# Performance work log

Measured on AMD Instinct MI355X. Metric: run time of the kernel, lower is better.

## Reference

```python
import jax, jax.numpy as jnp
import numpy as np

ORIENTATIONS = 9
CELL = 8  # pixels_per_cell


def setup_inputs() -> dict:
    key = jax.random.key(0)
    x = jax.random.normal(key, (64, 1, 512, 512), dtype=jnp.float32)
    base = jnp.array([[1.0, 0.0, -1.0], [2.0, 0.0, -2.0], [1.0, 0.0, -1.0]], dtype=jnp.float32)
    weight = jnp.stack([base, base.T])[:, None, :, :]  # [2,1,3,3]
    return {"x": x, "weight": weight}


def reference(x, weight):
    # 3x3 Sobel-like gradient conv (cross-correlation, padding=1), NCHW
    gxy = jax.lax.conv_general_dilated(
        x, weight, window_strides=(1, 1), padding=[(1, 1), (1, 1)],
        dimension_numbers=("NCHW", "OIHW", "NCHW"))  # [n,2,h,w]
    gx, gy = gxy[:, 0], gxy[:, 1]
    mag = jnp.sqrt(gx * gx + gy * gy)            # [n,h,w]
    phase = jnp.arctan2(gx, gy)                  # [n,h,w]
    phase_int = phase / jnp.pi * ORIENTATIONS
    fl = jnp.floor(phase_int).astype(jnp.int32) % ORIENTATIONS
    ce = jnp.ceil(phase_int).astype(jnp.int32) % ORIENTATIONS
    # scatter_(set into zeros) + scatter_add_ == sum of two weighted one-hots
    hist = (jax.nn.one_hot(fl, ORIENTATIONS, dtype=mag.dtype)
            + jax.nn.one_hot(ce, ORIENTATIONS, dtype=mag.dtype)) * mag[..., None]  # [n,h,w,O]
    out = jnp.transpose(hist, (0, 3, 1, 2))      # [n,O,h,w]
    n, o, h, w = out.shape
    # avg_pool2d with kernel==stride==CELL
    pooled = out.reshape(n, o, h // CELL, CELL, w // CELL, CELL).mean(axis=(3, 5))
    return pooled.reshape(n, -1)  # feature_vector=True
```

## Files before the change

### kernel.cpp

```cpp
#include <hip/hip_runtime.h>
#include <math.h>


#define IMH 512
#define IMW 512
#define NCELLS (64 * 64 * 64)

#define F32(h) __builtin_bit_cast(float, (unsigned)(h))
__device__ __forceinline__ unsigned fbits(float f) { return __builtin_bit_cast(unsigned, f); }
__device__ __forceinline__ int mod9(int b) { int r = b % 9; return r < 0 ? r + 9 : r; }

__device__ float fd_atanf_fma(float x) {
#pragma clang fp contract(off)
    unsigned hx = fbits(x);
    unsigned ix = hx & 0x7fffffffu;
    if (ix >= 0x4c800000u) {
        if (ix > 0x7f800000u) return x + x;
        float r = F32(0x3fc90fda) + F32(0x33a22168);
        return (hx >> 31) ? -r : r;
    }
    int id;
    if (ix < 0x3ee00000u) {
        if (ix < 0x39800000u) return x;
        id = -1;
    } else {
        x = fabsf(x);
        if (ix < 0x3f980000u) {
            if (ix < 0x3f300000u) { id = 0; x = fmaf(2.0f, x, -1.0f) / (2.0f + x); }
            else                  { id = 1; x = (x - 1.0f) / (x + 1.0f); }
        } else {
            if (ix < 0x401c0000u) { id = 2; x = (x - 1.5f) / fmaf(1.5f, x, 1.0f); }
            else                  { id = 3; x = -1.0f / x; }
        }
    }
    float z = x * x;
    float w = z * z;
    float s1 = z * fmaf(w, fmaf(w, F32(0x3d7cac25), F32(0x3e11f50d)), F32(0x3eaaaaa3));
    float s2 = w * fmaf(w, F32(0xbdda1247), F32(0xbe4cca98));
    if (id < 0) return fmaf(-x, s1 + s2, x);
    float hi = (id == 0) ? F32(0x3eed6338) : (id == 1) ? F32(0x3f490fda)
             : (id == 2) ? F32(0x3f7b985e) : F32(0x3fc90fda);
    float lo = (id == 0) ? F32(0x31ac3769) : (id == 1) ? F32(0x33222168)
             : (id == 2) ? F32(0x33140fb4) : F32(0x33a22168);
    float zz = hi - (fmaf(x, s1 + s2, -lo) - x);
    return (hx >> 31) ? -zz : zz;
}

__device__ float fd_atan2f_fma(float y, float x) {
#pragma clang fp contract(off)
    unsigned hx = fbits(x), hy = fbits(y);
    unsigned ix = hx & 0x7fffffffu, iy = hy & 0x7fffffffu;
    const float pi     = F32(0x40490fdb);
    const float pi_lo  = F32(0xb3bbbd2e);
    const float pi_o_2 = F32(0x3fc90fdb);
    if (hx == 0x3f800000u) return fd_atanf_fma(y);
    unsigned m = ((hy >> 31) & 1u) | ((hx >> 30) & 2u);
    if (iy == 0u) {
        switch (m) {
            case 0: case 1: return y;
            case 2: return pi;
            default: return -pi;
        }
    }
    if (ix == 0u) return (hy >> 31) ? -pi_o_2 : pi_o_2;
    int k = ((int)iy - (int)ix) >> 23;
    float z;
    unsigned mm = m;
    if (k > 26) {
        z = pi_o_2 + 0.5f * pi_lo;
        mm = m & 1u;
    } else if (k < -26 && (hx >> 31)) {
        z = 0.0f;
    } else {
        z = fd_atanf_fma(fabsf(y / x));
    }
    switch (mm) {
        case 0:  return z;
        case 1:  return -z;
        case 2:  return pi - (z - pi_lo);
        default: return (z - pi_lo) - pi;
    }
}

__global__ __launch_bounds__(256) void hog_kernel(const float* __restrict__ x,
                                                  float* __restrict__ out) {
#pragma clang fp contract(off)
    const int wid  = threadIdx.x >> 6;
    const int lane = threadIdx.x & 63;
    const int cell = blockIdx.x * 4 + wid;
    const int n  = cell >> 12;
    const int ch = (cell >> 6) & 63;
    const int cw = cell & 63;
    const int py = lane >> 3;
    const int px = lane & 7;
    const int h = (ch << 3) + py;
    const int w = (cw << 3) + px;

    const float* xn = x + (size_t)n * (IMH * IMW);

    float v[3][3];
#pragma unroll
    for (int dy = 0; dy < 3; ++dy) {
#pragma unroll
        for (int dx = 0; dx < 3; ++dx) {
            int hh = h + dy - 1;
            int ww = w + dx - 1;
            bool ok = ((unsigned)hh < (unsigned)IMH) && ((unsigned)ww < (unsigned)IMW);
            v[dy][dx] = ok ? xn[hh * IMW + ww] : 0.0f;
        }
    }

    float gx = v[0][0];
    gx = gx - v[0][2];
    gx = gx + 2.0f * v[1][0];
    gx = gx - 2.0f * v[1][2];
    gx = gx + v[2][0];
    gx = gx - v[2][2];

    float gy = v[0][0];
    gy = gy + 2.0f * v[0][1];
    gy = gy + v[0][2];
    gy = gy - v[2][0];
    gy = gy - 2.0f * v[2][1];
    gy = gy - v[2][2];

    float m2f = gx * gx + gy * gy;
    float mag = sqrtf(m2f);

    float Sx = fabsf(v[0][0]) + fabsf(v[0][2])
             + 2.0f * (fabsf(v[1][0]) + fabsf(v[1][2]))
             + fabsf(v[2][0]) + fabsf(v[2][2]);
    float Sy = fabsf(v[0][0]) + fabsf(v[2][0])
             + 2.0f * (fabsf(v[0][1]) + fabsf(v[2][1]))
             + fabsf(v[0][2]) + fabsf(v[2][2]);

    float ph32 = atan2f(gx, gy);
    float t32 = (ph32 / F32(0x40490fdb)) * 9.0f;
    float agx = fabsf(gx), agy = fabsf(gy);
    float Eph32 = 3.0e-7f * fabsf(ph32) + 1e-12f;
    if (m2f > 0.0f)
        Eph32 += (agy * (3.6e-7f * Sx) + agx * (3.6e-7f * Sy)) / m2f;
    float Et32 = 2.8648f * Eph32 + 3.6e-7f * fmaxf(fabsf(t32), 1.0f)
               + 3.5e-8f * fabsf(t32);
    float d32 = fabsf(t32 - rintf(t32));

    int b0 = 0, b1 = 0, b2 = 0;
    float w0 = 0.0f, w1 = 0.0f, w2 = 0.0f;

    if (d32 > 4.0f * Et32 && m2f > 0.0f) {
        int k0 = (int)floorf(t32);
        b0 = mod9(k0); b1 = mod9(k0 + 1);
        w0 = mag; w1 = mag;
    } else {
        double gx64 = ((double)v[0][0] - (double)v[0][2])
                    + 2.0 * ((double)v[1][0] - (double)v[1][2])
                    + ((double)v[2][0] - (double)v[2][2]);
        double gy64 = ((double)v[0][0] - (double)v[2][0])
                    + 2.0 * ((double)v[0][1] - (double)v[2][1])
                    + ((double)v[0][2] - (double)v[2][2]);
        double m2 = gx64 * gx64 + gy64 * gy64;
        if (m2 == 0.0) {
            b0 = 0; b1 = 0; w0 = mag; w1 = mag;
        } else {
            double ph = atan2(gx64, gy64);
            double t64 = (ph / 3.14159274101257324) * 9.0;
            double dgx = 2.4e-7 * (double)Sx;
            double dgy = 2.4e-7 * (double)Sy;
            double dpa = (fabs(gy64) * dgx + fabs(gx64) * dgy) / m2;
            double dpi = 2.4e-7 * fabs(ph) + 1e-30;
            double E = 2.86479 * (dpa + dpi)
                     + 1.8e-7 * fmax(fabs(t64), 1.0)
                     + 3.5e-8 * fabs(t64);
            double kd = floor(t64 + 0.5);
            double d = fabs(t64 - kd);
            int k = (int)kd;
            if (d <= E) {
                if (mag <= 8.3f) {
                    b0 = mod9(k - 1); b1 = mod9(k); b2 = mod9(k + 1);
                    w0 = 0.5f * mag; w1 = 1.5f * mag; w2 = 0.5f * mag;
                } else {
                    float phf = fd_atan2f_fma(gx, gy);
                    float tf = (phf / F32(0x40490fdb)) * 9.0f;
                    int fl = (int)floorf(tf);
                    int ce = (int)ceilf(tf);
                    b0 = mod9(fl); b1 = mod9(ce);
                    w0 = mag; w1 = mag;
                }
            } else {
                int k0 = (int)floor(t64);
                b0 = mod9(k0); b1 = mod9(k0 + 1);
                w0 = mag; w1 = mag;
            }
        }
    }

    float myband = 0.0f;
#pragma unroll
    for (int o = 0; o < 9; ++o) {
        float s = (b0 == o ? w0 : 0.0f) + (b1 == o ? w1 : 0.0f) + (b2 == o ? w2 : 0.0f);
#pragma unroll
        for (int d = 1; d < 64; d <<= 1) {
            s += __shfl_xor(s, d, 64);
        }
        if (lane == o) myband = s;
    }

    if (lane < 9) {
        out[(((size_t)n * 9 + lane) * 64 + ch) * 64 + cw] = myband * (1.0f / 64.0f);
    }
}

extern "C" void kernel_launch(void* const* d_in, const int* in_sizes, int n_in,
                              void* d_out, int out_size, void* d_ws, size_t ws_size,
                              hipStream_t stream) {
    const float* x = (const float*)d_in[0];
    float* out = (float*)d_out;
    const int blocks = NCELLS / 4;
    hog_kernel<<<blocks, 256, 0, stream>>>(x, out);
}
```

Before: 226.7 us.

## Stage input strips in LDS and accumulate cell histograms with shared atomics

```diff
diff --git a/kernel.cpp b/kernel.cpp
--- a/kernel.cpp
+++ b/kernel.cpp
@@ -4,7 +4,10 @@
 
 #define IMH 512
 #define IMW 512
-#define NCELLS (64 * 64 * 64)
+#define STRIP 32
+#define ROWS 10
+#define COLS (STRIP * 8 + 2)
+#define RS 261
 
 #define F32(h) __builtin_bit_cast(float, (unsigned)(h))
 __device__ __forceinline__ unsigned fbits(float f) { return __builtin_bit_cast(unsigned, f); }
@@ -85,128 +88,147 @@
 __global__ __launch_bounds__(256) void hog_kernel(const float* __restrict__ x,
                                                   float* __restrict__ out) {
 #pragma clang fp contract(off)
-    const int wid  = threadIdx.x >> 6;
-    const int lane = threadIdx.x & 63;
-    const int cell = blockIdx.x * 4 + wid;
-    const int n  = cell >> 12;
-    const int ch = (cell >> 6) & 63;
-    const int cw = cell & 63;
-    const int py = lane >> 3;
-    const int px = lane & 7;
-    const int h = (ch << 3) + py;
-    const int w = (cw << 3) + px;
+    __shared__ float tile[ROWS * RS];
+    __shared__ float hist[STRIP * 9];
+
+    const int tid = threadIdx.x;
+    const int bid = blockIdx.x;
+    const int n  = bid >> 7;
+    const int ch = (bid & 127) >> 1;
+    const int s  = bid & 1;
+    const int cw0px = s * (STRIP * 8);
 
     const float* xn = x + (size_t)n * (IMH * IMW);
 
-    float v[3][3];
-#pragma unroll
-    for (int dy = 0; dy < 3; ++dy) {
-#pragma unroll
-        for (int dx = 0; dx < 3; ++dx) {
-            int hh = h + dy - 1;
-            int ww = w + dx - 1;
-            bool ok = ((unsigned)hh < (unsigned)IMH) && ((unsigned)ww < (unsigned)IMW);
-            v[dy][dx] = ok ? xn[hh * IMW + ww] : 0.0f;
-        }
-    }
-
-    float gx = v[0][0];
-    gx = gx - v[0][2];
-    gx = gx + 2.0f * v[1][0];
-    gx = gx - 2.0f * v[1][2];
-    gx = gx + v[2][0];
-    gx = gx - v[2][2];
-
-    float gy = v[0][0];
-    gy = gy + 2.0f * v[0][1];
-    gy = gy + v[0][2];
-    gy = gy - v[2][0];
-    gy = gy - 2.0f * v[2][1];
-    gy = gy - v[2][2];
-
-    float m2f = gx * gx + gy * gy;
-    float mag = sqrtf(m2f);
-
-    float Sx = fabsf(v[0][0]) + fabsf(v[0][2])
-             + 2.0f * (fabsf(v[1][0]) + fabsf(v[1][2]))
-             + fabsf(v[2][0]) + fabsf(v[2][2]);
-    float Sy = fabsf(v[0][0]) + fabsf(v[2][0])
-             + 2.0f * (fabsf(v[0][1]) + fabsf(v[2][1]))
-             + fabsf(v[0][2]) + fabsf(v[2][2]);
-
-    float ph32 = atan2f(gx, gy);
-    float t32 = (ph32 / F32(0x40490fdb)) * 9.0f;
-    float agx = fabsf(gx), agy = fabsf(gy);
-    float Eph32 = 3.0e-7f * fabsf(ph32) + 1e-12f;
-    if (m2f > 0.0f)
-        Eph32 += (agy * (3.6e-7f * Sx) + agx * (3.6e-7f * Sy)) / m2f;
-    float Et32 = 2.8648f * Eph32 + 3.6e-7f * fmaxf(fabsf(t32), 1.0f)
-               + 3.5e-8f * fabsf(t32);
-    float d32 = fabsf(t32 - rintf(t32));
-
-    int b0 = 0, b1 = 0, b2 = 0;
-    float w0 = 0.0f, w1 = 0.0f, w2 = 0.0f;
-
-    if (d32 > 4.0f * Et32 && m2f > 0.0f) {
-        int k0 = (int)floorf(t32);
-        b0 = mod9(k0); b1 = mod9(k0 + 1);
-        w0 = mag; w1 = mag;
-    } else {
-        double gx64 = ((double)v[0][0] - (double)v[0][2])
-                    + 2.0 * ((double)v[1][0] - (double)v[1][2])
-                    + ((double)v[2][0] - (double)v[2][2]);
-        double gy64 = ((double)v[0][0] - (double)v[2][0])
-                    + 2.0 * ((double)v[0][1] - (double)v[2][1])
-                    + ((double)v[0][2] - (double)v[2][2]);
-        double m2 = gx64 * gx64 + gy64 * gy64;
-        if (m2 == 0.0) {
-            b0 = 0; b1 = 0; w0 = mag; w1 = mag;
+    for (int i = tid; i < STRIP * 9; i += 256) hist[i] = 0.0f;
+
+    const int gh0 = ch * 8 - 1;
+    const int gw0 = cw0px - 1;
+    for (int idx = tid; idx < ROWS * COLS; idx += 256) {
+        int row = idx / COLS;
+        int col = idx - row * COLS;
+        int gh = gh0 + row, gw = gw0 + col;
+        bool ok = ((unsigned)gh < (unsigned)IMH) && ((unsigned)gw < (unsigned)IMW);
+        tile[row * RS + col] = ok ? xn[gh * IMW + gw] : 0.0f;
+    }
+    __syncthreads();
+
+    const int c = tid >> 3;
+    const int r = tid & 7;
+    const float* t0 = &tile[(r + 0) * RS + c * 8];
+    const float* t1 = &tile[(r + 1) * RS + c * 8];
+    const float* t2 = &tile[(r + 2) * RS + c * 8];
+    float* hc = &hist[c * 9];
+
+    float a0 = t0[0], a1 = t0[1];
+    float b0 = t1[0], b1 = t1[1];
+    float cc0 = t2[0], cc1 = t2[1];
+
+    for (int px = 0; px < 8; ++px) {
+        float a2 = t0[px + 2];
+        float b2 = t1[px + 2];
+        float cc2 = t2[px + 2];
+
+        float gx = a0;
+        gx = gx - a2;
+        gx = gx + 2.0f * b0;
+        gx = gx - 2.0f * b2;
+        gx = gx + cc0;
+        gx = gx - cc2;
+
+        float gy = a0;
+        gy = gy + 2.0f * a1;
+        gy = gy + a2;
+        gy = gy - cc0;
+        gy = gy - 2.0f * cc1;
+        gy = gy - cc2;
+
+        float m2f = gx * gx + gy * gy;
+        float mag = sqrtf(m2f);
+
+        float Sx = fabsf(a0) + fabsf(a2)
+                 + 2.0f * (fabsf(b0) + fabsf(b2))
+                 + fabsf(cc0) + fabsf(cc2);
+        float Sy = fabsf(a0) + fabsf(cc0)
+                 + 2.0f * (fabsf(a1) + fabsf(cc1))
+                 + fabsf(a2) + fabsf(cc2);
+
+        float ph32 = atan2f(gx, gy);
+        float t32 = (ph32 / F32(0x40490fdb)) * 9.0f;
+        float agx = fabsf(gx), agy = fabsf(gy);
+        float Eph32 = 3.0e-7f * fabsf(ph32) + 1e-12f;
+        if (m2f > 0.0f)
+            Eph32 += (agy * (3.6e-7f * Sx) + agx * (3.6e-7f * Sy)) / m2f;
+        float Et32 = 2.8648f * Eph32 + 3.6e-7f * fmaxf(fabsf(t32), 1.0f)
+                   + 3.5e-8f * fabsf(t32);
+        float d32 = fabsf(t32 - rintf(t32));
+
+        int bn0 = 0, bn1 = 0, bn2 = 0;
+        float wt0 = 0.0f, wt1 = 0.0f, wt2 = 0.0f;
+
+        if (d32 > 4.0f * Et32 && m2f > 0.0f) {
+            int k0 = (int)floorf(t32);
+            bn0 = mod9(k0); bn1 = mod9(k0 + 1);
+            wt0 = mag; wt1 = mag;
         } else {
-            double ph = atan2(gx64, gy64);
-            double t64 = (ph / 3.14159274101257324) * 9.0;
-            double dgx = 2.4e-7 * (double)Sx;
-            double dgy = 2.4e-7 * (double)Sy;
-            double dpa = (fabs(gy64) * dgx + fabs(gx64) * dgy) / m2;
-            double dpi = 2.4e-7 * fabs(ph) + 1e-30;
-            double E = 2.86479 * (dpa + dpi)
-                     + 1.8e-7 * fmax(fabs(t64), 1.0)
-                     + 3.5e-8 * fabs(t64);
-            double kd = floor(t64 + 0.5);
-            double d = fabs(t64 - kd);
-            int k = (int)kd;
-            if (d <= E) {
-                if (mag <= 8.3f) {
-                    b0 = mod9(k - 1); b1 = mod9(k); b2 = mod9(k + 1);
-                    w0 = 0.5f * mag; w1 = 1.5f * mag; w2 = 0.5f * mag;
+            double gx64 = ((double)a0 - (double)a2)
+                        + 2.0 * ((double)b0 - (double)b2)
+                        + ((double)cc0 - (double)cc2);
+            double gy64 = ((double)a0 - (double)cc0)
+                        + 2.0 * ((double)a1 - (double)cc1)
+                        + ((double)a2 - (double)cc2);
+            double m2 = gx64 * gx64 + gy64 * gy64;
+            if (m2 == 0.0) {
+                bn0 = 0; bn1 = 0; wt0 = mag; wt1 = mag;
+            } else {
+                double ph = atan2(gx64, gy64);
+                double t64 = (ph / 3.14159274101257324) * 9.0;
+                double dgx = 2.4e-7 * (double)Sx;
+                double dgy = 2.4e-7 * (double)Sy;
+                double dpa = (fabs(gy64) * dgx + fabs(gx64) * dgy) / m2;
+                double dpi = 2.4e-7 * fabs(ph) + 1e-30;
+                double E = 2.86479 * (dpa + dpi)
+                         + 1.8e-7 * fmax(fabs(t64), 1.0)
+                         + 3.5e-8 * fabs(t64);
+                double kd = floor(t64 + 0.5);
+                double d = fabs(t64 - kd);
+                int k = (int)kd;
+                if (d <= E) {
+                    if (mag <= 8.3f) {
+                        bn0 = mod9(k - 1); bn1 = mod9(k); bn2 = mod9(k + 1);
+                        wt0 = 0.5f * mag; wt1 = 1.5f * mag; wt2 = 0.5f * mag;
+                    } else {
+                        float phf = fd_atan2f_fma(gx, gy);
+                        float tf = (phf / F32(0x40490fdb)) * 9.0f;
+                        int fl = (int)floorf(tf);
+                        int ce = (int)ceilf(tf);
+                        bn0 = mod9(fl); bn1 = mod9(ce);
+                        wt0 = mag; wt1 = mag;
+                    }
                 } else {
-                    float phf = fd_atan2f_fma(gx, gy);
-                    float tf = (phf / F32(0x40490fdb)) * 9.0f;
-                    int fl = (int)floorf(tf);
-                    int ce = (int)ceilf(tf);
-                    b0 = mod9(fl); b1 = mod9(ce);
-                    w0 = mag; w1 = mag;
+                    int k0 = (int)floor(t64);
+                    bn0 = mod9(k0); bn1 = mod9(k0 + 1);
+                    wt0 = mag; wt1 = mag;
                 }
-            } else {
-                int k0 = (int)floor(t64);
-                b0 = mod9(k0); b1 = mod9(k0 + 1);
-                w0 = mag; w1 = mag;
             }
         }
-    }
-
-    float myband = 0.0f;
-#pragma unroll
-    for (int o = 0; o < 9; ++o) {
-        float s = (b0 == o ? w0 : 0.0f) + (b1 == o ? w1 : 0.0f) + (b2 == o ? w2 : 0.0f);
-#pragma unroll
-        for (int d = 1; d < 64; d <<= 1) {
-            s += __shfl_xor(s, d, 64);
-        }
-        if (lane == o) myband = s;
-    }
-
-    if (lane < 9) {
-        out[(((size_t)n * 9 + lane) * 64 + ch) * 64 + cw] = myband * (1.0f / 64.0f);
+
+        atomicAdd(hc + bn0, wt0);
+        atomicAdd(hc + bn1, wt1);
+        if (wt2 != 0.0f) atomicAdd(hc + bn2, wt2);
+
+        a0 = a1; a1 = a2;
+        b0 = b1; b1 = b2;
+        cc0 = cc1; cc1 = cc2;
+    }
+
+    __syncthreads();
+
+    for (int i = tid; i < STRIP * 9; i += 256) {
+        int cc = i / 9;
+        int o  = i - cc * 9;
+        out[(((size_t)n * 9 + o) * 64 + ch) * 64 + (s * STRIP) + cc] =
+            hist[cc * 9 + o] * (1.0f / 64.0f);
     }
 }
 
@@ -215,6 +237,6 @@
                               hipStream_t stream) {
     const float* x = (const float*)d_in[0];
     float* out = (float*)d_out;
-    const int blocks = NCELLS / 4;
+    const int blocks = 64 * 64 * 2;
     hog_kernel<<<blocks, 256, 0, stream>>>(x, out);
 }
```

New measurement: 271.3 us. 1.2x slower.
